# Kernel optimization log

Hardware: AMD Instinct MI355X
Metric: run time of the kernel (lower is better)

Reference implementation:

```python
import jax, jax.numpy as jnp
import numpy as np

NUM_EMBEDDINGS = 8192
EMBEDDING_DIM = 128


def setup_inputs() -> dict:
    key = jax.random.key(0)
    k1, k2 = jax.random.split(key)
    inputs = jax.random.normal(k1, (8, 32, 32, EMBEDDING_DIM), dtype=jnp.float32)
    embedding_weight = jax.random.normal(k2, (NUM_EMBEDDINGS, EMBEDDING_DIM), dtype=jnp.float32)
    return {"inputs": inputs, "embedding_weight": embedding_weight}


def reference(inputs, embedding_weight):
    # inputs: [B, H, W, C] channels-last; embedding_weight: [K, C]
    input_shape = inputs.shape
    flat_input = inputs.reshape(-1, EMBEDDING_DIM)  # [N, C]

    distances = (
        jnp.sum(flat_input ** 2, axis=1, keepdims=True)
        + jnp.sum(embedding_weight ** 2, axis=1)
        - 2.0 * flat_input @ embedding_weight.T
    )
    encoding_indices = jnp.argmin(distances, axis=1)  # [N]

    # one-hot encodings (returned by the original module)
    encodings = jax.nn.one_hot(encoding_indices, NUM_EMBEDDINGS, dtype=jnp.float32)  # [N, K]

    # quantized via direct gather (same math as one_hot @ weight, no big matmul)
    quantized = embedding_weight[encoding_indices].reshape(input_shape)  # [B,H,W,C]

    # straight-through estimator
    quantized = inputs + jax.lax.stop_gradient(quantized - inputs)

    quantized_nchw = jnp.transpose(quantized, (0, 3, 1, 2))  # [B,C,H,W]
    return quantized_nchw, encodings
```

## Files before the change

### kernel.cpp

```cpp
#include <hip/hip_runtime.h>

typedef _Float16 f16x4 __attribute__((ext_vector_type(4)));
typedef _Float16 f16x8 __attribute__((ext_vector_type(8)));
typedef float    f32x16 __attribute__((ext_vector_type(16)));

#define HN_OFF   0u
#define BEST_OFF 32768u
#define EFH_OFF  98304u
#define EFL_OFF  (98304u + 2097152u)
#define XRH_OFF  (98304u + 2u * 2097152u)
#define XRL_OFF  (98304u + 3u * 2097152u)

#define OUT_ENC  1048576

__global__ __launch_bounds__(256) void k1_convert(const float* __restrict__ x,
                                                  const float* __restrict__ e,
                                                  char* __restrict__ wsb,
                                                  float* __restrict__ out) {
    int bx = blockIdx.x, tid = threadIdx.x;
    if (bx >= 1088) {
        int f = bx - 1088;
        float4* enc4 = (float4*)(out + OUT_ENC) + (size_t)f * 32768;
        float4 z4 = make_float4(0.f, 0.f, 0.f, 0.f);
        #pragma unroll
        for (int i = 0; i < 128; i++) enc4[i * 256 + tid] = z4;
        return;
    }
    if (bx < 64) {
        __shared__ f16x8 lds[4096];
        const float* src = e + (size_t)bx * 16384;
        float* hnp = (float*)(wsb + HN_OFF);
        #pragma unroll
        for (int it = 0; it < 8; it++) {
            int g = it * 256 + tid;
            int row = g >> 4, c16 = g & 15;
            float4 v0 = *(const float4*)(src + row * 128 + c16 * 8);
            float4 v1 = *(const float4*)(src + row * 128 + c16 * 8 + 4);
            float f[8] = {v0.x, v0.y, v0.z, v0.w, v1.x, v1.y, v1.z, v1.w};
            f16x8 hi, lo;
            float ss = 0.f;
            #pragma unroll
            for (int j = 0; j < 8; j++) {
                hi[j] = (_Float16)f[j];
                lo[j] = (_Float16)((f[j] - (float)hi[j]) * 2048.0f);
                ss += f[j] * f[j];
            }
            int sw = row ^ c16;
            lds[c16 * 128 + sw] = hi;
            lds[2048 + c16 * 128 + sw] = lo;
            #pragma unroll
            for (int o = 8; o > 0; o >>= 1) ss += __shfl_down(ss, o, 16);
            if ((tid & 15) == 0) hnp[bx * 128 + row] = 0.5f * ss;
        }
        __syncthreads();
        _Float16* eh = (_Float16*)(wsb + EFH_OFF);
        _Float16* el = (_Float16*)(wsb + EFL_OFF);
        #pragma unroll
        for (int it = 0; it < 16; it++) {
            int g = it * 256 + tid;
            int plane = g >> 11, gg = g & 2047;
            int chunk = gg >> 7, code = gg & 127;
            f16x8 v = lds[plane * 2048 + chunk * 128 + (code ^ chunk)];
            _Float16* dst = plane ? el : eh;
            *(f16x8*)(dst + ((size_t)bx * 2048 + gg) * 8) = v;
        }
    } else {
        int sec = bx - 64;
        size_t off = (size_t)sec * 1024 + tid * 4;
        float4 v = *(const float4*)(x + off);
        f16x4 hi, lo;
        hi[0] = (_Float16)v.x; hi[1] = (_Float16)v.y;
        hi[2] = (_Float16)v.z; hi[3] = (_Float16)v.w;
        lo[0] = (_Float16)((v.x - (float)hi[0]) * 2048.0f);
        lo[1] = (_Float16)((v.y - (float)hi[1]) * 2048.0f);
        lo[2] = (_Float16)((v.z - (float)hi[2]) * 2048.0f);
        lo[3] = (_Float16)((v.w - (float)hi[3]) * 2048.0f);
        *(f16x4*)((_Float16*)(wsb + XRH_OFF) + off) = hi;
        *(f16x4*)((_Float16*)(wsb + XRL_OFF) + off) = lo;
        if (sec < 32)
            ((unsigned long long*)(wsb + BEST_OFF))[sec * 256 + tid] = 0ull;
    }
}

__global__ __launch_bounds__(256, 2) void k2_mfma(char* __restrict__ wsb) {
    __shared__ _Float16 lds_eh[128 * 128];
    __shared__ _Float16 lds_el[128 * 128];
    __shared__ float    lds_hn[1024];

    const _Float16* xrh = (const _Float16*)(wsb + XRH_OFF);
    const _Float16* xrl = (const _Float16*)(wsb + XRL_OFF);
    const _Float16* erh = (const _Float16*)(wsb + EFH_OFF);
    const _Float16* erl = (const _Float16*)(wsb + EFL_OFF);
    const float* hn = (const float*)(wsb + HN_OFF);
    unsigned long long* bestg = (unsigned long long*)(wsb + BEST_OFF);

    int tid = threadIdx.x;
    int lane = tid & 63, wave = tid >> 6;
    int col = lane & 31, half = lane >> 5;
    int bx = blockIdx.x, by = blockIdx.y;
    int r0 = bx * 128;
    int k0g = by * 1024;
    int row = r0 + wave * 32 + col;

    f16x8 ah[8], al[8];
    #pragma unroll
    for (int s = 0; s < 8; s++) {
        ah[s] = *(const f16x8*)(xrh + (size_t)row * 128 + s * 16 + half * 8);
        al[s] = *(const f16x8*)(xrl + (size_t)row * 128 + s * 16 + half * 8);
    }

    *(float4*)(lds_hn + tid * 4) = *(const float4*)(hn + k0g + tid * 4);

    float best[16];
    int bidx[16];
    #pragma unroll
    for (int i = 0; i < 16; i++) { best[i] = -3.0e38f; bidx[i] = 0; }

    for (int kt = 0; kt < 8; kt++) {
        __syncthreads();
        const f16x8* sh = (const f16x8*)erh + ((size_t)(by * 8 + kt) * 2048);
        const f16x8* sl = (const f16x8*)erl + ((size_t)(by * 8 + kt) * 2048);
        #pragma unroll
        for (int i = 0; i < 16; i++) {
            int g = tid + i * 256;
            int gg = g & 2047;
            int chunk = gg >> 7, code = gg & 127;
            f16x8 v = (i < 8) ? sh[gg] : sl[gg];
            _Float16* dstp = (i < 8) ? lds_eh : lds_el;
            *(f16x8*)(dstp + code * 128 + ((chunk ^ (code & 15)) * 8)) = v;
        }
        __syncthreads();

        #pragma unroll
        for (int sub = 0; sub < 4; sub++) {
            f32x16 a0, a1, a2;
            #pragma unroll
            for (int i = 0; i < 16; i++) { a0[i] = 0.f; a1[i] = 0.f; a2[i] = 0.f; }
            int cbase = (sub * 32 + col) * 128;
            #pragma unroll
            for (int s = 0; s < 8; s++) {
                int so = ((s * 2 + half) ^ (col & 15)) * 8;
                f16x8 bh = *(const f16x8*)(lds_eh + cbase + so);
                f16x8 bl = *(const f16x8*)(lds_el + cbase + so);
                a0 = __builtin_amdgcn_mfma_f32_32x32x16_f16(ah[s], bh, a0, 0, 0, 0);
                a1 = __builtin_amdgcn_mfma_f32_32x32x16_f16(ah[s], bl, a1, 0, 0, 0);
                a2 = __builtin_amdgcn_mfma_f32_32x32x16_f16(al[s], bh, a2, 0, 0, 0);
            }
            int code = k0g + kt * 128 + sub * 32 + col;
            float hnv = lds_hn[kt * 128 + sub * 32 + col];
            #pragma unroll
            for (int r = 0; r < 16; r++) {
                float sc = a0[r] + (a1[r] + a2[r]) * (1.0f / 2048.0f) - hnv;
                if (sc > best[r]) { best[r] = sc; bidx[r] = code; }
            }
        }
    }

    #pragma unroll
    for (int r = 0; r < 16; r++) {
        float s = best[r];
        int bi = bidx[r];
        #pragma unroll
        for (int m = 1; m < 32; m <<= 1) {
            float qs = __shfl_xor(s, m, 64);
            int qi = __shfl_xor(bi, m, 64);
            if (qs > s || (qs == s && qi < bi)) { s = qs; bi = qi; }
        }
        if (col == 0) {
            int rl = (r & 3) + 8 * (r >> 2) + 4 * half;
            unsigned ub = __float_as_uint(s);
            ub = ((int)ub < 0) ? ~ub : (ub | 0x80000000u);
            unsigned long long p = ((unsigned long long)ub << 32) |
                                   (unsigned long long)(0xFFFFFFFFu - (unsigned)bi);
            atomicMax(&bestg[r0 + wave * 32 + rl], p);
        }
    }
}

__global__ __launch_bounds__(256) void k3_final(const char* __restrict__ wsb,
                                                const float* __restrict__ wgt,
                                                float* __restrict__ out) {
    int n = blockIdx.x * 256 + threadIdx.x;
    unsigned long long p = ((const unsigned long long*)(wsb + BEST_OFF))[n];
    int bi = (int)(0xFFFFFFFFu - (unsigned)(p & 0xFFFFFFFFull));

    out[(size_t)OUT_ENC + (size_t)n * 8192 + bi] = 1.0f;

    int bq = n >> 10, hw = n & 1023;
    float* o = out + (size_t)bq * 131072 + hw;
    const float4* wrow = (const float4*)(wgt + (size_t)bi * 128);
    #pragma unroll
    for (int c4 = 0; c4 < 32; c4++) {
        float4 v = wrow[c4];
        o[(c4 * 4 + 0) * 1024] = v.x;
        o[(c4 * 4 + 1) * 1024] = v.y;
        o[(c4 * 4 + 2) * 1024] = v.z;
        o[(c4 * 4 + 3) * 1024] = v.w;
    }
}

extern "C" void kernel_launch(void* const* d_in, const int* in_sizes, int n_in,
                              void* d_out, int out_size, void* d_ws, size_t ws_size,
                              hipStream_t stream) {
    const float* x = (const float*)d_in[0];
    const float* e = (const float*)d_in[1];
    float* out = (float*)d_out;
    char* ws = (char*)d_ws;

    k1_convert<<<1600, 256, 0, stream>>>(x, e, ws, out);
    k2_mfma<<<dim3(64, 8), 256, 0, stream>>>(ws);
    k3_final<<<32, 256, 0, stream>>>(ws, e, out);
}
```

Before: 362.4 us.

## Pre-swizzle codebook in global and stream tiles via direct global-to-LDS loads

The codebook conversion now writes f16 hi/lo tiles already in the swizzled LDS layout, so the MFMA kernel can copy them straight into shared memory with global_load_lds instead of going through registers. The per-code half-norm table is read from global memory instead of being staged in LDS. The one-hot zero fill moves out of the convert kernel into its own launch. This cuts register traffic and LDS staging work in the hot kernel, at the cost of an extra kernel launch and uncached scalar-ish global reads of the norms.

```diff
diff --git a/kernel.cpp b/kernel.cpp
--- a/kernel.cpp
+++ b/kernel.cpp
@@ -3,6 +3,9 @@
 typedef _Float16 f16x4 __attribute__((ext_vector_type(4)));
 typedef _Float16 f16x8 __attribute__((ext_vector_type(8)));
 typedef float    f32x16 __attribute__((ext_vector_type(16)));
+
+typedef const __attribute__((address_space(1))) unsigned int gu32;
+typedef __attribute__((address_space(3))) unsigned int su32;
 
 #define HN_OFF   0u
 #define BEST_OFF 32768u
@@ -13,19 +16,17 @@
 
 #define OUT_ENC  1048576
 
+__global__ __launch_bounds__(256) void k0_fill(float* __restrict__ out) {
+    float4* enc4 = (float4*)(out + OUT_ENC) + (size_t)blockIdx.x * 32768;
+    float4 z4 = make_float4(0.f, 0.f, 0.f, 0.f);
+    #pragma unroll
+    for (int i = 0; i < 128; i++) enc4[i * 256 + threadIdx.x] = z4;
+}
+
 __global__ __launch_bounds__(256) void k1_convert(const float* __restrict__ x,
                                                   const float* __restrict__ e,
-                                                  char* __restrict__ wsb,
-                                                  float* __restrict__ out) {
+                                                  char* __restrict__ wsb) {
     int bx = blockIdx.x, tid = threadIdx.x;
-    if (bx >= 1088) {
-        int f = bx - 1088;
-        float4* enc4 = (float4*)(out + OUT_ENC) + (size_t)f * 32768;
-        float4 z4 = make_float4(0.f, 0.f, 0.f, 0.f);
-        #pragma unroll
-        for (int i = 0; i < 128; i++) enc4[i * 256 + tid] = z4;
-        return;
-    }
     if (bx < 64) {
         __shared__ f16x8 lds[4096];
         const float* src = e + (size_t)bx * 16384;
@@ -62,7 +63,8 @@
             int chunk = gg >> 7, code = gg & 127;
             f16x8 v = lds[plane * 2048 + chunk * 128 + (code ^ chunk)];
             _Float16* dst = plane ? el : eh;
-            *(f16x8*)(dst + ((size_t)bx * 2048 + gg) * 8) = v;
+            int dstg = code * 16 + (chunk ^ (code & 15));
+            *(f16x8*)(dst + ((size_t)bx * 2048 + dstg) * 8) = v;
         }
     } else {
         int sec = bx - 64;
@@ -85,12 +87,11 @@
 __global__ __launch_bounds__(256, 2) void k2_mfma(char* __restrict__ wsb) {
     __shared__ _Float16 lds_eh[128 * 128];
     __shared__ _Float16 lds_el[128 * 128];
-    __shared__ float    lds_hn[1024];
 
     const _Float16* xrh = (const _Float16*)(wsb + XRH_OFF);
     const _Float16* xrl = (const _Float16*)(wsb + XRL_OFF);
-    const _Float16* erh = (const _Float16*)(wsb + EFH_OFF);
-    const _Float16* erl = (const _Float16*)(wsb + EFL_OFF);
+    const char* erh = (const char*)(wsb + EFH_OFF);
+    const char* erl = (const char*)(wsb + EFL_OFF);
     const float* hn = (const float*)(wsb + HN_OFF);
     unsigned long long* bestg = (unsigned long long*)(wsb + BEST_OFF);
 
@@ -109,8 +110,6 @@
         al[s] = *(const f16x8*)(xrl + (size_t)row * 128 + s * 16 + half * 8);
     }
 
-    *(float4*)(lds_hn + tid * 4) = *(const float4*)(hn + k0g + tid * 4);
-
     float best[16];
     int bidx[16];
     #pragma unroll
@@ -118,16 +117,19 @@
 
     for (int kt = 0; kt < 8; kt++) {
         __syncthreads();
-        const f16x8* sh = (const f16x8*)erh + ((size_t)(by * 8 + kt) * 2048);
-        const f16x8* sl = (const f16x8*)erl + ((size_t)(by * 8 + kt) * 2048);
-        #pragma unroll
-        for (int i = 0; i < 16; i++) {
-            int g = tid + i * 256;
-            int gg = g & 2047;
-            int chunk = gg >> 7, code = gg & 127;
-            f16x8 v = (i < 8) ? sh[gg] : sl[gg];
-            _Float16* dstp = (i < 8) ? lds_eh : lds_el;
-            *(f16x8*)(dstp + code * 128 + ((chunk ^ (code & 15)) * 8)) = v;
+        {
+            const char* sh = erh + (size_t)(by * 8 + kt) * 32768;
+            const char* sl = erl + (size_t)(by * 8 + kt) * 32768;
+            #pragma unroll
+            for (int i = 0; i < 8; i++) {
+                int g = tid + i * 256;
+                __builtin_amdgcn_global_load_lds(
+                    (gu32*)(sh + (size_t)g * 16),
+                    (su32*)((char*)lds_eh + (size_t)g * 16), 16, 0, 0);
+                __builtin_amdgcn_global_load_lds(
+                    (gu32*)(sl + (size_t)g * 16),
+                    (su32*)((char*)lds_el + (size_t)g * 16), 16, 0, 0);
+            }
         }
         __syncthreads();
 
@@ -147,7 +149,7 @@
                 a2 = __builtin_amdgcn_mfma_f32_32x32x16_f16(al[s], bh, a2, 0, 0, 0);
             }
             int code = k0g + kt * 128 + sub * 32 + col;
-            float hnv = lds_hn[kt * 128 + sub * 32 + col];
+            float hnv = hn[code];
             #pragma unroll
             for (int r = 0; r < 16; r++) {
                 float sc = a0[r] + (a1[r] + a2[r]) * (1.0f / 2048.0f) - hnv;
@@ -207,7 +209,8 @@
     float* out = (float*)d_out;
     char* ws = (char*)d_ws;
 
-    k1_convert<<<1600, 256, 0, stream>>>(x, e, ws, out);
+    k0_fill<<<512, 256, 0, stream>>>(out);
+    k1_convert<<<1088, 256, 0, stream>>>(x, e, ws);
     k2_mfma<<<dim3(64, 8), 256, 0, stream>>>(ws);
     k3_final<<<32, 256, 0, stream>>>(ws, e, out);
 }
```

Result: faster. 347.1 us (-4.2%).
